# Kernel optimization log

Measured on AMD Instinct MI355X. Metric: run time of the kernel, lower is better.

The kernel has to match this reference:

```python
import jax, jax.numpy as jnp
import numpy as np
from jax import lax

H_STARLET = jnp.array([1/16, 1/4, 3/8, 1/4, 1/16], dtype=jnp.float32)
N_SCALES = 4

def _wav_filter():
    # outer product of the 1D starlet filter -> [5,5,1,1] HWIO
    f = jnp.outer(H_STARLET, H_STARLET)
    return f[:, :, None, None]

def _analysis(image, filt, n_scales):
    """Undecimated starlet analysis: per scale, symmetric-pad, dilated conv,
    subtract. Returns list of high-freq coeffs (each same shape as image)."""
    low = image
    coeffs = []
    half = H_STARLET.shape[0] // 2  # len(filter)//2 == 2
    for i_scale in range(n_scales):
        dil = 2 ** i_scale
        p = half * dil
        padded = jnp.pad(low, ((0, 0), (p, p), (p, p), (0, 0)), mode='symmetric')
        new_low = lax.conv_general_dilated(
            padded, filt, window_strides=(1, 1), padding='VALID',
            rhs_dilation=(dil, dil),
            dimension_numbers=('NHWC', 'HWIO', 'NHWC'))
        coeffs.append(low - new_low)
        low = new_low
    return coeffs, low

def setup_inputs() -> dict:
    key = jax.random.key(0)
    k_img, k_noise = jax.random.split(key)
    image = jax.random.normal(k_img, (16, 1024, 1024, 1), dtype=jnp.float32)
    # Replicate __init__ normalization: std of each wavelet coeff of white noise.
    filt = _wav_filter()
    noise = jax.random.normal(k_noise, (1, 1024, 1024, 1), dtype=jnp.float32)
    noise_coeffs, _ = _analysis(noise, filt, N_SCALES)
    wav_norms = jnp.stack([jnp.std(c) for c in noise_coeffs])  # [n_scales]
    return {"image": image, "wav_norms": wav_norms}

def reference(image, wav_norms):
    filt = _wav_filter()
    coeffs, _ = _analysis(image, filt, N_SCALES)
    coeffs = [c / wav_norms[i] for i, c in enumerate(coeffs)]
    # coarse=False: only the n_scales high-frequency bands are returned.
    # All have identical shape (undecimated) -> stack: [n_scales, B, H, W, 1]
    return jnp.stack(coeffs)
```

## Files before the change

kernel.cpp:

```cpp
#include <hip/hip_runtime.h>


#define IMG_H 1024
#define IMG_W 1024
#define NBATCH 16
#define TILE 64

__device__ __forceinline__ int mirror_idx(int g, int n) {
    g = (g < 0) ? (-1 - g) : g;
    g = (g >= n) ? (2 * n - 1 - g) : g;
    return g;
}

template <int DIL>
__global__ __launch_bounds__(256)
void starlet_scale_kernel(const float* __restrict__ low_in,
                          const float* __restrict__ norms,
                          float* __restrict__ coeff_out,
                          float* __restrict__ low_out,
                          int scale)
{
    constexpr int R  = 2 * DIL;
    constexpr int R2 = TILE + 2 * R;
    __shared__ float lowbuf[R2 * R2];
    __shared__ float tmp[R2 * TILE];

    const int tid = threadIdx.x;
    const int tx0 = blockIdx.x * TILE;
    const int ty0 = blockIdx.y * TILE;
    const size_t img_off = (size_t)blockIdx.z * (size_t)(IMG_H * IMG_W);
    const float inv = 1.0f / norms[scale];

    for (int i = tid; i < R2 * R2; i += 256) {
        const int ry = i / R2;
        const int rx = i - ry * R2;
        const int gy = mirror_idx(ty0 - R + ry, IMG_H);
        const int gx = mirror_idx(tx0 - R + rx, IMG_W);
        lowbuf[i] = low_in[img_off + (size_t)gy * IMG_W + gx];
    }
    __syncthreads();

    for (int i = tid; i < R2 * TILE; i += 256) {
        const int y = i >> 6;
        const int x = i & (TILE - 1);
        const float* row = &lowbuf[y * R2 + x + R];
        tmp[i] = 0.375f  * row[0]
               + 0.25f   * (row[-DIL]     + row[DIL])
               + 0.0625f * (row[-2 * DIL] + row[2 * DIL]);
    }
    __syncthreads();

    for (int i = tid; i < TILE * TILE; i += 256) {
        const int y = i >> 6;
        const int x = i & (TILE - 1);
        const float* col = &tmp[(y + R) * TILE + x];
        const float nl = 0.375f  * col[0]
                       + 0.25f   * (col[-DIL * TILE]     + col[DIL * TILE])
                       + 0.0625f * (col[-2 * DIL * TILE] + col[2 * DIL * TILE]);
        const float lo = lowbuf[(y + R) * R2 + (x + R)];
        const size_t go = img_off + (size_t)(ty0 + y) * IMG_W + (tx0 + x);
        coeff_out[go] = (lo - nl) * inv;
        if (low_out) low_out[go] = nl;
    }
}

extern "C" void kernel_launch(void* const* d_in, const int* in_sizes, int n_in,
                              void* d_out, int out_size, void* d_ws, size_t ws_size,
                              hipStream_t stream) {
    const float* image = (const float*)d_in[0];
    const float* norms = (const float*)d_in[1];
    float* out = (float*)d_out;

    const size_t plane = (size_t)NBATCH * IMG_H * IMG_W;
    float* wsA = (float*)d_ws;
    float* wsB = wsA + plane;

    dim3 grid(IMG_W / TILE, IMG_H / TILE, NBATCH);
    dim3 block(256);

    starlet_scale_kernel<1><<<grid, block, 0, stream>>>(image, norms, out,             wsA,     0);
    starlet_scale_kernel<2><<<grid, block, 0, stream>>>(wsA,   norms, out + plane,     wsB,     1);
    starlet_scale_kernel<4><<<grid, block, 0, stream>>>(wsB,   norms, out + 2 * plane, wsA,     2);
    starlet_scale_kernel<8><<<grid, block, 0, stream>>>(wsA,   norms, out + 3 * plane, nullptr, 3);
}
```

Before: 454.6 us.

## Fuse all four starlet scales into one kernel with a wide shared-memory halo

Replaces four per-scale launches with a single kernel that loads a 124x124 tile (halo 30) once and computes all dilated scales in shared memory with shrinking valid regions. This removes the global writes and reads of intermediate low-pass planes and three launches. It also vectorises the passes with float4. In exchange it does redundant halo computation, uses about 137KB of LDS with 1024-thread blocks, and so limits occupancy.

```diff
diff --git a/kernel.cpp b/kernel.cpp
--- a/kernel.cpp
+++ b/kernel.cpp
@@ -1,10 +1,14 @@
 #include <hip/hip_runtime.h>
 
 
-#define IMG_H 1024
-#define IMG_W 1024
+#define IMG    1024
 #define NBATCH 16
-#define TILE 64
+#define TILE   64
+#define RTOT   30
+#define SA     (TILE + 2 * RTOT)
+#define BS     1024
+
+static_assert(SA == 124, "halo arithmetic");
 
 __device__ __forceinline__ int mirror_idx(int g, int n) {
     g = (g < 0) ? (-1 - g) : g;
@@ -12,56 +16,149 @@
     return g;
 }
 
-template <int DIL>
-__global__ __launch_bounds__(256)
-void starlet_scale_kernel(const float* __restrict__ low_in,
-                          const float* __restrict__ norms,
-                          float* __restrict__ coeff_out,
-                          float* __restrict__ low_out,
-                          int scale)
+__device__ __forceinline__ float4 tap5(float4 q0, float4 q1, float4 q2,
+                                       float4 q3, float4 q4) {
+    float4 o;
+    o.x = 0.375f * q2.x + 0.25f * (q1.x + q3.x) + 0.0625f * (q0.x + q4.x);
+    o.y = 0.375f * q2.y + 0.25f * (q1.y + q3.y) + 0.0625f * (q0.y + q4.y);
+    o.z = 0.375f * q2.z + 0.25f * (q1.z + q3.z) + 0.0625f * (q0.z + q4.z);
+    o.w = 0.375f * q2.w + 0.25f * (q1.w + q3.w) + 0.0625f * (q0.w + q4.w);
+    return o;
+}
+
+template <int D, int NIN>
+__device__ __forceinline__ void h_pass(const float* __restrict__ A,
+                                       float* __restrict__ B, int tid) {
+    constexpr int NOUT = NIN - 4 * D;
+    constexpr int GX = NOUT / 4;
+    for (int t = tid; t < NIN * GX; t += BS) {
+        const int y = t / GX;
+        const int x = (t - y * GX) * 4;
+        const float* row = &A[y * SA + x];
+        float4 o;
+        if constexpr (D == 1) {
+            const float4 a = *(const float4*)(row);
+            const float4 b = *(const float4*)(row + 4);
+            o = tap5(a,
+                     make_float4(a.y, a.z, a.w, b.x),
+                     make_float4(a.z, a.w, b.x, b.y),
+                     make_float4(a.w, b.x, b.y, b.z),
+                     b);
+        } else if constexpr (D == 2) {
+            const float4 a = *(const float4*)(row);
+            const float4 b = *(const float4*)(row + 4);
+            const float4 c = *(const float4*)(row + 8);
+            o = tap5(a,
+                     make_float4(a.z, a.w, b.x, b.y),
+                     b,
+                     make_float4(b.z, b.w, c.x, c.y),
+                     c);
+        } else {
+            o = tap5(*(const float4*)(row),
+                     *(const float4*)(row + D),
+                     *(const float4*)(row + 2 * D),
+                     *(const float4*)(row + 3 * D),
+                     *(const float4*)(row + 4 * D));
+        }
+        *(float4*)(&B[y * NOUT + x]) = o;
+    }
+}
+
+template <int NIN>
+__device__ __forceinline__ void copy_central(const float* __restrict__ A,
+                                             float* __restrict__ S, int tid) {
+    constexpr int PMIN = (NIN - TILE) / 2;
+    for (int t = tid; t < TILE * TILE; t += BS) {
+        const int sy = t >> 6;
+        const int sx = t & (TILE - 1);
+        S[t] = A[(PMIN + sy) * SA + (PMIN + sx)];
+    }
+}
+
+template <int D, int NIN, bool LAST>
+__device__ __forceinline__ void v_pass(float* __restrict__ A,
+                                       const float* __restrict__ B,
+                                       const float* __restrict__ S,
+                                       float* __restrict__ gout, size_t img_off,
+                                       int ty0, int tx0, float inv, int tid) {
+    constexpr int NOUT = NIN - 4 * D;
+    constexpr int GX = NOUT / 4;
+    constexpr int CMIN = (NOUT - TILE) / 2;
+    for (int t = tid; t < NOUT * GX; t += BS) {
+        const int y = t / GX;
+        const int x = (t - y * GX) * 4;
+        const float* col = &B[y * NOUT + x];
+        const float4 nl = tap5(*(const float4*)(col),
+                               *(const float4*)(col + D * NOUT),
+                               *(const float4*)(col + 2 * D * NOUT),
+                               *(const float4*)(col + 3 * D * NOUT),
+                               *(const float4*)(col + 4 * D * NOUT));
+        if constexpr (!LAST) {
+            *(float4*)(&A[y * SA + x]) = nl;
+        }
+        if (y >= CMIN && y < CMIN + TILE && x >= CMIN && x < CMIN + TILE) {
+            const int sy = y - CMIN, sx = x - CMIN;
+            const float4 lo = *(const float4*)(&S[sy * TILE + sx]);
+            float4 cf;
+            cf.x = (lo.x - nl.x) * inv;
+            cf.y = (lo.y - nl.y) * inv;
+            cf.z = (lo.z - nl.z) * inv;
+            cf.w = (lo.w - nl.w) * inv;
+            *(float4*)(&gout[img_off + (size_t)(ty0 + sy) * IMG + (tx0 + sx)]) = cf;
+        }
+    }
+}
+
+__global__ __launch_bounds__(BS)
+void starlet_fused(const float* __restrict__ img, const float* __restrict__ norms,
+                   float* __restrict__ out)
 {
-    constexpr int R  = 2 * DIL;
-    constexpr int R2 = TILE + 2 * R;
-    __shared__ float lowbuf[R2 * R2];
-    __shared__ float tmp[R2 * TILE];
+    __shared__ float A[SA * SA];
+    __shared__ float B[SA * (SA - 4)];
+    __shared__ float S[TILE * TILE];
 
     const int tid = threadIdx.x;
     const int tx0 = blockIdx.x * TILE;
     const int ty0 = blockIdx.y * TILE;
-    const size_t img_off = (size_t)blockIdx.z * (size_t)(IMG_H * IMG_W);
-    const float inv = 1.0f / norms[scale];
+    const size_t img_off = (size_t)blockIdx.z * (size_t)(IMG * IMG);
+    const size_t plane = (size_t)NBATCH * IMG * IMG;
 
-    for (int i = tid; i < R2 * R2; i += 256) {
-        const int ry = i / R2;
-        const int rx = i - ry * R2;
-        const int gy = mirror_idx(ty0 - R + ry, IMG_H);
-        const int gx = mirror_idx(tx0 - R + rx, IMG_W);
-        lowbuf[i] = low_in[img_off + (size_t)gy * IMG_W + gx];
+    const float i0 = 1.0f / norms[0];
+    const float i1 = 1.0f / norms[1];
+    const float i2 = 1.0f / norms[2];
+    const float i3 = 1.0f / norms[3];
+
+    for (int i = tid; i < SA * SA; i += BS) {
+        const int ry = i / SA;
+        const int rx = i - ry * SA;
+        const int gy = mirror_idx(ty0 - RTOT + ry, IMG);
+        const int gx = mirror_idx(tx0 - RTOT + rx, IMG);
+        A[i] = img[img_off + (size_t)gy * IMG + gx];
     }
     __syncthreads();
 
-    for (int i = tid; i < R2 * TILE; i += 256) {
-        const int y = i >> 6;
-        const int x = i & (TILE - 1);
-        const float* row = &lowbuf[y * R2 + x + R];
-        tmp[i] = 0.375f  * row[0]
-               + 0.25f   * (row[-DIL]     + row[DIL])
-               + 0.0625f * (row[-2 * DIL] + row[2 * DIL]);
-    }
+    h_pass<1, 124>(A, B, tid);
+    copy_central<124>(A, S, tid);
+    __syncthreads();
+    v_pass<1, 124, false>(A, B, S, out, img_off, ty0, tx0, i0, tid);
     __syncthreads();
 
-    for (int i = tid; i < TILE * TILE; i += 256) {
-        const int y = i >> 6;
-        const int x = i & (TILE - 1);
-        const float* col = &tmp[(y + R) * TILE + x];
-        const float nl = 0.375f  * col[0]
-                       + 0.25f   * (col[-DIL * TILE]     + col[DIL * TILE])
-                       + 0.0625f * (col[-2 * DIL * TILE] + col[2 * DIL * TILE]);
-        const float lo = lowbuf[(y + R) * R2 + (x + R)];
-        const size_t go = img_off + (size_t)(ty0 + y) * IMG_W + (tx0 + x);
-        coeff_out[go] = (lo - nl) * inv;
-        if (low_out) low_out[go] = nl;
-    }
+    h_pass<2, 120>(A, B, tid);
+    copy_central<120>(A, S, tid);
+    __syncthreads();
+    v_pass<2, 120, false>(A, B, S, out + plane, img_off, ty0, tx0, i1, tid);
+    __syncthreads();
+
+    h_pass<4, 112>(A, B, tid);
+    copy_central<112>(A, S, tid);
+    __syncthreads();
+    v_pass<4, 112, false>(A, B, S, out + 2 * plane, img_off, ty0, tx0, i2, tid);
+    __syncthreads();
+
+    h_pass<8, 96>(A, B, tid);
+    copy_central<96>(A, S, tid);
+    __syncthreads();
+    v_pass<8, 96, true>(A, B, S, out + 3 * plane, img_off, ty0, tx0, i3, tid);
 }
 
 extern "C" void kernel_launch(void* const* d_in, const int* in_sizes, int n_in,
@@ -71,15 +168,6 @@
     const float* norms = (const float*)d_in[1];
     float* out = (float*)d_out;
 
-    const size_t plane = (size_t)NBATCH * IMG_H * IMG_W;
-    float* wsA = (float*)d_ws;
-    float* wsB = wsA + plane;
-
-    dim3 grid(IMG_W / TILE, IMG_H / TILE, NBATCH);
-    dim3 block(256);
-
-    starlet_scale_kernel<1><<<grid, block, 0, stream>>>(image, norms, out,             wsA,     0);
-    starlet_scale_kernel<2><<<grid, block, 0, stream>>>(wsA,   norms, out + plane,     wsB,     1);
-    starlet_scale_kernel<4><<<grid, block, 0, stream>>>(wsB,   norms, out + 2 * plane, wsA,     2);
-    starlet_scale_kernel<8><<<grid, block, 0, stream>>>(wsA,   norms, out + 3 * plane, nullptr, 3);
+    dim3 grid(IMG / TILE, IMG / TILE, NBATCH);
+    starlet_fused<<<grid, dim3(BS), 0, stream>>>(image, norms, out);
 }
```

New measurement: 453.8 us. Within noise of the previous version (-0.2%).
